# Kernel optimization log

Hardware: AMD Instinct MI355X
Metric: run time of the kernel (lower is better)

Reference implementation:

```python
import jax, jax.numpy as jnp
import numpy as np

N = 40000   # input nodes
M = 40000   # output nodes
DEG = 16    # fixed degree -> row_splits = arange(M+1)*DEG
E = M * DEG
B = 2
C = 128     # out_channels == feature channels
H = 128     # hidden_dim
P = 3       # positional dim per node (in_channels)


def setup_inputs() -> dict:
    key = jax.random.key(0)
    k = jax.random.split(key, 8)
    x_in = jax.random.normal(k[0], (N, P), dtype=jnp.float32)
    x_out = jax.random.normal(k[1], (M, P), dtype=jnp.float32)
    in_features = jax.random.normal(k[2], (B, N, C), dtype=jnp.float32)
    neighbor_idx = jax.random.randint(k[3], (E,), 0, N)
    row_splits = jnp.arange(M + 1, dtype=jnp.int32) * DEG
    W1 = jax.random.normal(k[4], (2 * P, H), dtype=jnp.float32) / np.sqrt(2 * P)
    b1 = jnp.zeros((H,), dtype=jnp.float32)
    W2 = jax.random.normal(k[5], (H, C), dtype=jnp.float32) / np.sqrt(H)
    b2 = jnp.zeros((C,), dtype=jnp.float32)
    return {"x_in": x_in, "x_out": x_out, "in_features": in_features,
            "neighbor_idx": neighbor_idx, "row_splits": row_splits,
            "W1": W1, "b1": b1, "W2": W2, "b2": b2}


def reference(x_in, x_out, in_features, neighbor_idx, row_splits, W1, b1, W2, b2):
    e = neighbor_idx.shape[0]
    m = row_splits.shape[0] - 1
    num_reps = row_splits[1:] - row_splits[:-1]               # [M]
    rep_feats = x_in[neighbor_idx]                            # [E, P] gather source coords
    gathered = in_features[:, neighbor_idx]                   # [B, E, C]
    self_feats = jnp.repeat(x_out, num_reps, axis=0, total_repeat_length=e)  # [E, P]
    agg = jnp.concatenate([rep_feats, self_feats], axis=1)    # [E, 2P]
    h = jax.nn.gelu(agg @ W1 + b1, approximate=False)         # torch.nn.GELU = exact erf gelu
    msg = h @ W2 + b2                                         # [E, C]
    weighted = msg[None, :, :] * gathered                     # [B, E, C]
    seg_ids = jnp.repeat(jnp.arange(m), num_reps, total_repeat_length=e)      # [E]
    sums = jax.ops.segment_sum(jnp.transpose(weighted, (1, 0, 2)), seg_ids, num_segments=m)  # [M, B, C]
    counts = jnp.maximum(num_reps, 1).astype(sums.dtype)      # segment_csr 'mean'
    out = sums / counts[:, None, None]                        # [M, B, C]
    return jnp.transpose(out, (1, 0, 2))                      # [B, M, C]
```

## Files before the change

kernel.cpp:

```cpp
#include <hip/hip_runtime.h>
#include <hip/hip_bf16.h>

#define CC 128
#define HH 128
#define NB 8

typedef __attribute__((ext_vector_type(8))) _Float16 half8;
typedef __attribute__((ext_vector_type(2))) _Float16 half2v;
typedef __attribute__((ext_vector_type(2))) __fp16   fp16x2;
typedef __attribute__((ext_vector_type(4))) float f32x4;

union H2U { half2v h; fp16x2 g; unsigned int u; };

__device__ __forceinline__ unsigned int pkrtz(float a, float b) {
    H2U v; v.g = __builtin_amdgcn_cvt_pkrtz(a, b); return v.u;
}

__device__ __forceinline__ float gelu_f(float x) {
    float x2 = x * x;
    float t  = fmaf(0.044715f, x2, 1.0f);
    float a  = x * t;
    float e  = __builtin_amdgcn_exp2f(a * 2.3022092f);
    float r  = __builtin_amdgcn_rcpf(e + 1.0f);
    return fmaf(-x, r, x);
}

__global__ __launch_bounds__(256)
void f32_to_f16_kernel(const float* __restrict__ in,
                       _Float16* __restrict__ out, long n8) {
    long i = (long)blockIdx.x * blockDim.x + threadIdx.x;
    const long stride = (long)gridDim.x * blockDim.x;
    for (; i < n8; i += stride) {
        const float4* p = reinterpret_cast<const float4*>(in) + i * 2;
        float4 a = p[0], b = p[1];
        half8 o;
        o[0] = (_Float16)a.x; o[1] = (_Float16)a.y;
        o[2] = (_Float16)a.z; o[3] = (_Float16)a.w;
        o[4] = (_Float16)b.x; o[5] = (_Float16)b.y;
        o[6] = (_Float16)b.z; o[7] = (_Float16)b.w;
        *reinterpret_cast<half8*>(out + i * 8) = o;
    }
}

template<bool F16G>
__global__ __launch_bounds__(512, 4)
void nmlp_kernel(const float* __restrict__ x_in,
                 const float* __restrict__ x_out,
                 const float* __restrict__ in_feat,
                 const _Float16* __restrict__ gws,
                 const int* __restrict__ nbr,
                 const int* __restrict__ row_splits,
                 const float* __restrict__ W1,
                 const float* __restrict__ b1,
                 const float* __restrict__ W2,
                 const float* __restrict__ b2,
                 float* __restrict__ out,
                 int N, int M)
{
    __shared__ __align__(16) char hb[NB * 16 * 256];
    __shared__ __align__(16) char msgb[NB * 16 * 256];
    __shared__ __align__(16) char aggb[NB * 16 * 16];
    __shared__ int ids_lds[NB * 16];

    const int tid  = threadIdx.x;
    const int lane = tid & 63;
    const int wave = tid >> 6;
    const int cbase = wave * 16;
    const int l15  = lane & 15;
    const int kgrp = lane >> 4;

    half8 w1frag;
    #pragma unroll
    for (int i = 0; i < 8; ++i) {
        int k = kgrp*8 + i;
        w1frag[i] = (k < 6) ? (_Float16)W1[k*HH + cbase + l15] : (_Float16)0.f;
    }
    half8 bfrag[4];
    #pragma unroll
    for (int kb = 0; kb < 4; ++kb)
        #pragma unroll
        for (int i = 0; i < 8; ++i) {
            int k = kb*32 + kgrp*8 + i;
            bfrag[kb][i] = (_Float16)W2[k*CC + cbase + l15];
        }
    float b1v[4], b2v[4];
    #pragma unroll
    for (int i = 0; i < 4; ++i) {
        b1v[i] = b1[cbase + kgrp*4 + i];
        b2v[i] = b2[cbase + kgrp*4 + i];
    }

    const _Float16* g0p = gws;
    const _Float16* g1p = gws + (size_t)N * CC;
    const float* f0p = in_feat;
    const float* f1p = in_feat + (size_t)N * CC;

    const int arow_off = l15 * 256;
    const int aswz = (l15 & 7) << 4;
    const int wcol_off = (cbase + kgrp*4) * 2;

    const int bb     = lane >> 5;
    const int ehalf  = (lane >> 4) & 1;
    const int cchunk = lane & 15;

    const int ngroups = (M + NB - 1) / NB;
    for (int g = blockIdx.x; g < ngroups; g += gridDim.x) {
        const int m0 = g * NB;

        if (tid < NB*16) {
            const int r = tid >> 4, e = tid & 15;
            const int m = m0 + r;
            int id = 0; int dg = 0;
            if (m < M) { int s = row_splits[m]; dg = row_splits[m+1] - s;
                         if (e < dg) id = nbr[s + e]; }
            const bool valid = (m < M) && (e < dg);
            ids_lds[tid] = id;
            float a0=0.f,a1=0.f,a2=0.f,a3=0.f,a4=0.f,a5=0.f;
            if (valid) {
                a0 = x_in[id*3+0]; a1 = x_in[id*3+1]; a2 = x_in[id*3+2];
                a3 = x_out[m*3+0]; a4 = x_out[m*3+1]; a5 = x_out[m*3+2];
            }
            uint4 pk;
            pk.x = pkrtz(a0, a1);
            pk.y = pkrtz(a2, a3);
            pk.z = pkrtz(a4, a5);
            pk.w = 0u;
            *reinterpret_cast<uint4*>(&aggb[tid*16]) = pk;
        }
        __syncthreads();

        uint4 gv[8];
        if (F16G) {
            const _Float16* gp = bb ? g1p : g0p;
            #pragma unroll
            for (int e8 = 0; e8 < 8; ++e8) {
                const int id = ids_lds[wave*16 + ehalf*8 + e8];
                gv[e8] = *reinterpret_cast<const uint4*>(
                    gp + (size_t)id*CC + cchunk*8);
            }
        }

        #pragma unroll
        for (int r = 0; r < NB; ++r) {
            half8 af;
            #pragma unroll
            for (int i = 0; i < 8; ++i) af[i] = (_Float16)0.f;
            if (kgrp == 0)
                af = *reinterpret_cast<const half8*>(&aggb[(r*16 + l15)*16]);
            f32x4 pa = {0.f, 0.f, 0.f, 0.f};
            pa = __builtin_amdgcn_mfma_f32_16x16x32_f16(w1frag, af, pa, 0, 0, 0);
            float g0 = gelu_f(pa[0] + b1v[0]);
            float g1 = gelu_f(pa[1] + b1v[1]);
            float g2 = gelu_f(pa[2] + b1v[2]);
            float g3 = gelu_f(pa[3] + b1v[3]);
            uint2 w = make_uint2(pkrtz(g0, g1), pkrtz(g2, g3));
            *reinterpret_cast<uint2*>(
                hb + r*4096 + l15*256 + (wcol_off ^ aswz)) = w;
        }
        __syncthreads();

        #pragma unroll
        for (int r = 0; r < NB; ++r) {
            f32x4 a = {0.f, 0.f, 0.f, 0.f};
            const char* base = hb + r*4096 + arow_off;
            #pragma unroll
            for (int kb = 0; kb < 4; ++kb) {
                half8 hf = *reinterpret_cast<const half8*>(
                    base + ((kb*64 + kgrp*16) ^ aswz));
                a = __builtin_amdgcn_mfma_f32_16x16x32_f16(bfrag[kb], hf, a, 0, 0, 0);
            }
            uint2 w = make_uint2(pkrtz(a[0] + b2v[0], a[1] + b2v[1]),
                                 pkrtz(a[2] + b2v[2], a[3] + b2v[3]));
            *reinterpret_cast<uint2*>(
                msgb + r*4096 + l15*256 + (wcol_off ^ aswz)) = w;
        }
        __syncthreads();

        const int m = m0 + wave;
        if (m < M) {
            const int dg = row_splits[m+1] - row_splits[m];
            half2v o0 = {0,0}, o1 = {0,0}, o2 = {0,0}, o3 = {0,0};
            #pragma unroll
            for (int e8 = 0; e8 < 8; ++e8) {
                const int e = ehalf*8 + e8;
                if (e < dg) {
                    const uint4 mv = *reinterpret_cast<const uint4*>(
                        msgb + wave*4096 + e*256 + ((cchunk*16) ^ ((e & 7) << 4)));
                    uint4 gvv;
                    if (F16G) {
                        gvv = gv[e8];
                    } else {
                        const float* fp = bb ? f1p : f0p;
                        const int id = ids_lds[wave*16 + e];
                        const float4* q = reinterpret_cast<const float4*>(
                            fp + (size_t)id*CC + cchunk*8);
                        float4 qa = q[0], qb = q[1];
                        gvv.x = pkrtz(qa.x, qa.y); gvv.y = pkrtz(qa.z, qa.w);
                        gvv.z = pkrtz(qb.x, qb.y); gvv.w = pkrtz(qb.z, qb.w);
                    }
                    H2U ma, ga;
                    ma.u = mv.x; ga.u = gvv.x; o0 += ma.h * ga.h;
                    ma.u = mv.y; ga.u = gvv.y; o1 += ma.h * ga.h;
                    ma.u = mv.z; ga.u = gvv.z; o2 += ma.h * ga.h;
                    ma.u = mv.w; ga.u = gvv.w; o3 += ma.h * ga.h;
                }
            }
            H2U u0, u1, u2, u3, p;
            u0.h = o0; u1.h = o1; u2.h = o2; u3.h = o3;
            p.u = (unsigned int)__shfl_xor((int)u0.u, 16); u0.h += p.h;
            p.u = (unsigned int)__shfl_xor((int)u1.u, 16); u1.h += p.h;
            p.u = (unsigned int)__shfl_xor((int)u2.u, 16); u2.h += p.h;
            p.u = (unsigned int)__shfl_xor((int)u3.u, 16); u3.h += p.h;
            if (ehalf == 0) {
                const float invd = 1.f / (float)(dg > 0 ? dg : 1);
                float* op = out + (size_t)bb*M*CC + (size_t)m*CC + cchunk*8;
                float4 v0 = {(float)u0.h[0]*invd, (float)u0.h[1]*invd,
                             (float)u1.h[0]*invd, (float)u1.h[1]*invd};
                float4 v1 = {(float)u2.h[0]*invd, (float)u2.h[1]*invd,
                             (float)u3.h[0]*invd, (float)u3.h[1]*invd};
                *reinterpret_cast<float4*>(op)     = v0;
                *reinterpret_cast<float4*>(op + 4) = v1;
            }
        }
        __syncthreads();
    }
}

extern "C" void kernel_launch(void* const* d_in, const int* in_sizes, int n_in,
                              void* d_out, int out_size, void* d_ws, size_t ws_size,
                              hipStream_t stream) {
    const float* x_in    = (const float*)d_in[0];
    const float* x_out   = (const float*)d_in[1];
    const float* in_feat = (const float*)d_in[2];
    const int*   nbr     = (const int*)d_in[3];
    const int*   rs      = (const int*)d_in[4];
    const float* W1      = (const float*)d_in[5];
    const float* b1      = (const float*)d_in[6];
    const float* W2      = (const float*)d_in[7];
    const float* b2      = (const float*)d_in[8];
    float* out = (float*)d_out;

    const int N = in_sizes[0] / 3;
    const int M = in_sizes[1] / 3;

    const int ngroups = (M + NB - 1) / NB;
    int grid = ngroups < 1024 ? ngroups : 1024;

    const size_t nfeat = (size_t)2 * N * CC;
    const bool use_f16 = (ws_size >= nfeat * sizeof(_Float16)) &&
                         (nfeat % 8 == 0);
    if (use_f16) {
        const long n8 = (long)(nfeat / 8);
        int cgrid = (int)((n8 + 255) / 256);
        if (cgrid > 4096) cgrid = 4096;
        f32_to_f16_kernel<<<cgrid, 256, 0, stream>>>(
            in_feat, (_Float16*)d_ws, n8);
        nmlp_kernel<true><<<grid, 512, 0, stream>>>(
            x_in, x_out, in_feat, (const _Float16*)d_ws,
            nbr, rs, W1, b1, W2, b2, out, N, M);
    } else {
        nmlp_kernel<false><<<grid, 512, 0, stream>>>(
            x_in, x_out, in_feat, nullptr,
            nbr, rs, W1, b1, W2, b2, out, N, M);
    }
}
```

Before: 89.04 us.

## Issue neighbor-feature gathers before LDS staging and fold biases into MFMA accumulators

Each wave now loads its own neighbor indices straight from global memory (vectorized int4 when degree is 16) and issues the f16 feature gathers at the top of the group iteration, before the sync and MLP stages. This lets the gather latency overlap the MLP compute and drops the ids LDS buffer. Biases are used as the initial MFMA accumulators instead of being added afterward, and there is a specialized unguarded path for degree 16. The grid is also halved to 512 blocks. The trade-off is higher register pressure from holding the gathered values across the MLP phases.

```diff
diff --git a/kernel.cpp b/kernel.cpp
--- a/kernel.cpp
+++ b/kernel.cpp
@@ -60,7 +60,6 @@
     __shared__ __align__(16) char hb[NB * 16 * 256];
     __shared__ __align__(16) char msgb[NB * 16 * 256];
     __shared__ __align__(16) char aggb[NB * 16 * 16];
-    __shared__ int ids_lds[NB * 16];
 
     const int tid  = threadIdx.x;
     const int lane = tid & 63;
@@ -102,10 +101,37 @@
     const int bb     = lane >> 5;
     const int ehalf  = (lane >> 4) & 1;
     const int cchunk = lane & 15;
+    const _Float16* gpb = bb ? g1p : g0p;
 
     const int ngroups = (M + NB - 1) / NB;
     for (int g = blockIdx.x; g < ngroups; g += gridDim.x) {
         const int m0 = g * NB;
+        const int mw = m0 + wave;
+
+        int sW = 0, dgv = 0;
+        if (mw < M) { sW = row_splits[mw]; dgv = row_splits[mw+1] - sW; }
+        const int dgs = __builtin_amdgcn_readfirstlane(dgv);
+        int ids8[8];
+        if (dgs == 16 && ((sW & 3) == 0)) {
+            const int4 ia = *reinterpret_cast<const int4*>(nbr + sW + ehalf*8);
+            const int4 ib = *reinterpret_cast<const int4*>(nbr + sW + ehalf*8 + 4);
+            ids8[0]=ia.x; ids8[1]=ia.y; ids8[2]=ia.z; ids8[3]=ia.w;
+            ids8[4]=ib.x; ids8[5]=ib.y; ids8[6]=ib.z; ids8[7]=ib.w;
+        } else {
+            #pragma unroll
+            for (int e8 = 0; e8 < 8; ++e8) {
+                const int e = ehalf*8 + e8;
+                ids8[e8] = (e < dgs) ? nbr[sW + e] : 0;
+            }
+        }
+        uint4 gv[8];
+        if (F16G) {
+            const _Float16* gcp = gpb + cchunk*8;
+            #pragma unroll
+            for (int e8 = 0; e8 < 8; ++e8)
+                gv[e8] = *reinterpret_cast<const uint4*>(
+                    gcp + (size_t)ids8[e8]*CC);
+        }
 
         if (tid < NB*16) {
             const int r = tid >> 4, e = tid & 15;
@@ -114,7 +140,6 @@
             if (m < M) { int s = row_splits[m]; dg = row_splits[m+1] - s;
                          if (e < dg) id = nbr[s + e]; }
             const bool valid = (m < M) && (e < dg);
-            ids_lds[tid] = id;
             float a0=0.f,a1=0.f,a2=0.f,a3=0.f,a4=0.f,a5=0.f;
             if (valid) {
                 a0 = x_in[id*3+0]; a1 = x_in[id*3+1]; a2 = x_in[id*3+2];
@@ -129,30 +154,15 @@
         }
         __syncthreads();
 
-        uint4 gv[8];
-        if (F16G) {
-            const _Float16* gp = bb ? g1p : g0p;
-            #pragma unroll
-            for (int e8 = 0; e8 < 8; ++e8) {
-                const int id = ids_lds[wave*16 + ehalf*8 + e8];
-                gv[e8] = *reinterpret_cast<const uint4*>(
-                    gp + (size_t)id*CC + cchunk*8);
-            }
-        }
-
         #pragma unroll
         for (int r = 0; r < NB; ++r) {
-            half8 af;
-            #pragma unroll
-            for (int i = 0; i < 8; ++i) af[i] = (_Float16)0.f;
-            if (kgrp == 0)
-                af = *reinterpret_cast<const half8*>(&aggb[(r*16 + l15)*16]);
-            f32x4 pa = {0.f, 0.f, 0.f, 0.f};
+            half8 af = *reinterpret_cast<const half8*>(&aggb[(r*16 + l15)*16]);
+            f32x4 pa = {b1v[0], b1v[1], b1v[2], b1v[3]};
             pa = __builtin_amdgcn_mfma_f32_16x16x32_f16(w1frag, af, pa, 0, 0, 0);
-            float g0 = gelu_f(pa[0] + b1v[0]);
-            float g1 = gelu_f(pa[1] + b1v[1]);
-            float g2 = gelu_f(pa[2] + b1v[2]);
-            float g3 = gelu_f(pa[3] + b1v[3]);
+            float g0 = gelu_f(pa[0]);
+            float g1 = gelu_f(pa[1]);
+            float g2 = gelu_f(pa[2]);
+            float g3 = gelu_f(pa[3]);
             uint2 w = make_uint2(pkrtz(g0, g1), pkrtz(g2, g3));
             *reinterpret_cast<uint2*>(
                 hb + r*4096 + l15*256 + (wcol_off ^ aswz)) = w;
@@ -161,7 +171,7 @@
 
         #pragma unroll
         for (int r = 0; r < NB; ++r) {
-            f32x4 a = {0.f, 0.f, 0.f, 0.f};
+            f32x4 a = {b2v[0], b2v[1], b2v[2], b2v[3]};
             const char* base = hb + r*4096 + arow_off;
             #pragma unroll
             for (int kb = 0; kb < 4; ++kb) {
@@ -169,40 +179,60 @@
                     base + ((kb*64 + kgrp*16) ^ aswz));
                 a = __builtin_amdgcn_mfma_f32_16x16x32_f16(bfrag[kb], hf, a, 0, 0, 0);
             }
-            uint2 w = make_uint2(pkrtz(a[0] + b2v[0], a[1] + b2v[1]),
-                                 pkrtz(a[2] + b2v[2], a[3] + b2v[3]));
+            uint2 w = make_uint2(pkrtz(a[0], a[1]), pkrtz(a[2], a[3]));
             *reinterpret_cast<uint2*>(
                 msgb + r*4096 + l15*256 + (wcol_off ^ aswz)) = w;
         }
         __syncthreads();
 
-        const int m = m0 + wave;
-        if (m < M) {
-            const int dg = row_splits[m+1] - row_splits[m];
+        if (mw < M) {
             half2v o0 = {0,0}, o1 = {0,0}, o2 = {0,0}, o3 = {0,0};
-            #pragma unroll
-            for (int e8 = 0; e8 < 8; ++e8) {
-                const int e = ehalf*8 + e8;
-                if (e < dg) {
+            const char* mbase = msgb + wave*4096;
+            if (dgs == 16) {
+                #pragma unroll
+                for (int e8 = 0; e8 < 8; ++e8) {
+                    const int e = ehalf*8 + e8;
                     const uint4 mv = *reinterpret_cast<const uint4*>(
-                        msgb + wave*4096 + e*256 + ((cchunk*16) ^ ((e & 7) << 4)));
-                    uint4 gvv;
-                    if (F16G) {
-                        gvv = gv[e8];
-                    } else {
+                        mbase + e*256 + ((cchunk*16) ^ ((e & 7) << 4)));
+                    const uint4 gvv = F16G ? gv[e8] : uint4{0,0,0,0};
+                    uint4 gq = gvv;
+                    if (!F16G) {
                         const float* fp = bb ? f1p : f0p;
-                        const int id = ids_lds[wave*16 + e];
                         const float4* q = reinterpret_cast<const float4*>(
-                            fp + (size_t)id*CC + cchunk*8);
+                            fp + (size_t)ids8[e8]*CC + cchunk*8);
                         float4 qa = q[0], qb = q[1];
-                        gvv.x = pkrtz(qa.x, qa.y); gvv.y = pkrtz(qa.z, qa.w);
-                        gvv.z = pkrtz(qb.x, qb.y); gvv.w = pkrtz(qb.z, qb.w);
+                        gq.x = pkrtz(qa.x, qa.y); gq.y = pkrtz(qa.z, qa.w);
+                        gq.z = pkrtz(qb.x, qb.y); gq.w = pkrtz(qb.z, qb.w);
                     }
                     H2U ma, ga;
-                    ma.u = mv.x; ga.u = gvv.x; o0 += ma.h * ga.h;
-                    ma.u = mv.y; ga.u = gvv.y; o1 += ma.h * ga.h;
-                    ma.u = mv.z; ga.u = gvv.z; o2 += ma.h * ga.h;
-                    ma.u = mv.w; ga.u = gvv.w; o3 += ma.h * ga.h;
+                    ma.u = mv.x; ga.u = gq.x; o0 += ma.h * ga.h;
+                    ma.u = mv.y; ga.u = gq.y; o1 += ma.h * ga.h;
+                    ma.u = mv.z; ga.u = gq.z; o2 += ma.h * ga.h;
+                    ma.u = mv.w; ga.u = gq.w; o3 += ma.h * ga.h;
+                }
+            } else {
+                #pragma unroll
+                for (int e8 = 0; e8 < 8; ++e8) {
+                    const int e = ehalf*8 + e8;
+                    if (e < dgs) {
+                        const uint4 mv = *reinterpret_cast<const uint4*>(
+                            mbase + e*256 + ((cchunk*16) ^ ((e & 7) << 4)));
+                        uint4 gq;
+                        if (F16G) gq = gv[e8];
+                        else {
+                            const float* fp = bb ? f1p : f0p;
+                            const float4* q = reinterpret_cast<const float4*>(
+                                fp + (size_t)ids8[e8]*CC + cchunk*8);
+                            float4 qa = q[0], qb = q[1];
+                            gq.x = pkrtz(qa.x, qa.y); gq.y = pkrtz(qa.z, qa.w);
+                            gq.z = pkrtz(qb.x, qb.y); gq.w = pkrtz(qb.z, qb.w);
+                        }
+                        H2U ma, ga;
+                        ma.u = mv.x; ga.u = gq.x; o0 += ma.h * ga.h;
+                        ma.u = mv.y; ga.u = gq.y; o1 += ma.h * ga.h;
+                        ma.u = mv.z; ga.u = gq.z; o2 += ma.h * ga.h;
+                        ma.u = mv.w; ga.u = gq.w; o3 += ma.h * ga.h;
+                    }
                 }
             }
             H2U u0, u1, u2, u3, p;
@@ -212,8 +242,9 @@
             p.u = (unsigned int)__shfl_xor((int)u2.u, 16); u2.h += p.h;
             p.u = (unsigned int)__shfl_xor((int)u3.u, 16); u3.h += p.h;
             if (ehalf == 0) {
-                const float invd = 1.f / (float)(dg > 0 ? dg : 1);
-                float* op = out + (size_t)bb*M*CC + (size_t)m*CC + cchunk*8;
+                const float invd = (dgs == 16) ? 0.0625f
+                                 : 1.f / (float)(dgs > 0 ? dgs : 1);
+                float* op = out + (size_t)bb*M*CC + (size_t)mw*CC + cchunk*8;
                 float4 v0 = {(float)u0.h[0]*invd, (float)u0.h[1]*invd,
                              (float)u1.h[0]*invd, (float)u1.h[1]*invd};
                 float4 v1 = {(float)u2.h[0]*invd, (float)u2.h[1]*invd,
@@ -244,7 +275,7 @@
     const int M = in_sizes[1] / 3;
 
     const int ngroups = (M + NB - 1) / NB;
-    int grid = ngroups < 1024 ? ngroups : 1024;
+    int grid = ngroups < 512 ? ngroups : 512;
 
     const size_t nfeat = (size_t)2 * N * CC;
     const bool use_f16 = (ws_size >= nfeat * sizeof(_Float16)) &&
```

After: 90.23 us. No clear change (+1.3%).
